# Performance work log

Measured on AMD Instinct MI355X. Metric: run time of the kernel, lower is better.

Reference implementation:

```python
import jax, jax.numpy as jnp
import numpy as np

B, N, FEAT, HID, HEADS = 16, 1024, 512, 1024, 2

def setup_inputs() -> dict:
    key = jax.random.key(0)
    ks = jax.random.split(key, 20)
    s = 0.03
    d = {
        'Fs':  jax.random.normal(ks[0], (B, N, FEAT), jnp.float32),
        'Fq':  jax.random.normal(ks[1], (B, N, FEAT), jnp.float32),
        'Fms': jax.random.normal(ks[2], (B, N, FEAT), jnp.float32),
        'out_dim': N,
        'W1': jax.random.normal(ks[3], (FEAT, FEAT), jnp.float32) * s,
        'W2': jax.random.normal(ks[4], (FEAT, FEAT), jnp.float32) * s,
        'W3': jax.random.normal(ks[5], (FEAT, FEAT), jnp.float32) * s,
        'W4': jax.random.normal(ks[6], (FEAT, FEAT), jnp.float32) * s,
        'W5': jax.random.normal(ks[7], (FEAT, FEAT), jnp.float32) * s,
        'W6': jax.random.normal(ks[8], (FEAT, FEAT), jnp.float32) * s,
        'Wq': jax.random.normal(ks[9], (N, N), jnp.float32) * s,
        'Wk': jax.random.normal(ks[10], (N, N), jnp.float32) * s,
        'Wv': jax.random.normal(ks[11], (N, N), jnp.float32) * s,
        'ln_g': jnp.ones((N,), jnp.float32),
        'ln_b': jnp.zeros((N,), jnp.float32),
        'ffn_w1': jax.random.normal(ks[12], (N, HID), jnp.float32) * s,
        'ffn_w2': jax.random.normal(ks[13], (HID, N), jnp.float32) * s,
        'ffn_ln_g': jnp.ones((N,), jnp.float32),
        'ffn_ln_b': jnp.zeros((N,), jnp.float32),
    }
    return d

def _layernorm(x, g, b, eps):
    mu = x.mean(-1, keepdims=True)
    var = x.var(-1, keepdims=True)
    return (x - mu) * jax.lax.rsqrt(var + eps) * g + b

def _affinity(a, b, Wa, Wb, cl):
    # softmax((a Wa)(b Wb)^T / sqrt(cl)) over last axis
    s = jnp.einsum('bnc,bmc->bnm', a @ Wa, b @ Wb) / jnp.sqrt(jnp.float32(cl))
    return jax.nn.softmax(s, axis=-1)

def reference(Fs, Fq, Fms, out_dim, W1, W2, W3, W4, W5, W6, Wq, Wk, Wv,
              ln_g, ln_b, ffn_w1, ffn_w2, ffn_ln_g, ffn_ln_b):
    ass = _affinity(Fms, Fms, W1, W2, Fms.shape[2])   # [B,N,N]
    asq = _affinity(Fs, Fq, W3, W4, Fs.shape[2])      # [B,N,N]
    aqq = _affinity(Fq, Fq, W5, W6, Fq.shape[2])      # [B,N,N]

    Q, K, V = asq @ Wq, ass @ Wk, asq @ Wv            # [B,N,C], C=N
    Bb, Nn, C = Q.shape
    g = C // HEADS
    def heads(x):
        return x.reshape(Bb, Nn, HEADS, g).transpose(0, 2, 1, 3)  # [B,h,N,g]
    Qs, Ks, Vs = heads(Q), heads(K), heads(V)
    attn = jax.nn.softmax(jnp.einsum('bhqg,bhkg->bhqk', Qs, Ks) / jnp.sqrt(jnp.float32(g)), axis=-1)
    o = jnp.einsum('bhqk,bhkg->bhqg', attn, Vs)
    o = o.transpose(0, 2, 1, 3).reshape(Bb, Nn, C)

    x = _layernorm(o + aqq, ln_g, ln_b, 1e-5)
    y = jnp.maximum(x @ ffn_w1, 0.0) @ ffn_w2 + x     # dropout = identity (eval)
    y = _layernorm(y, ffn_ln_g, ffn_ln_b, 1e-6)
    return y
```

## Files before the change

kernel.cpp:

```cpp
#include <hip/hip_runtime.h>
#include <cstdint>

static constexpr long long Bb = 16, Nn = 1024, FE = 512;
static constexpr long long BN = Bb * Nn;
static constexpr long long E1e = BN * FE;
static constexpr long long E2n = BN * Nn;

static constexpr long long O_WT  = 0;
static constexpr long long SZ_W512 = FE * FE * 2;
static constexpr long long O_WQT = O_WT + 6 * SZ_W512;
static constexpr long long SZ_W1K = Nn * Nn * 2;
static constexpr long long O_WKT = O_WQT + SZ_W1K;
static constexpr long long O_WVT = O_WKT + SZ_W1K;
static constexpr long long O_F1T = O_WVT + SZ_W1K;
static constexpr long long O_F2T = O_F1T + SZ_W1K;
static constexpr long long O_SLOTS = O_F2T + SZ_W1K;
static constexpr long long SLOT = E2n * 2;
static constexpr long long O_S0 = O_SLOTS;
static constexpr long long O_S1 = O_S0 + SLOT;
static constexpr long long O_S2 = O_S1 + SLOT;
static constexpr long long O_E0 = O_S2 + SLOT;
static constexpr long long O_E1 = O_E0 + SLOT;
static constexpr long long O_E2 = O_E1 + SLOT;
static constexpr long long WS_NEED = O_E2 + SLOT;
static constexpr long long O_FMSB = O_E1;
static constexpr long long O_FSB  = O_E1 + E1e * 2;
static constexpr long long O_FQB  = O_E2;
static constexpr long long O_C2   = O_E2 + E1e * 2;

typedef __attribute__((ext_vector_type(8))) short short8;
typedef __attribute__((ext_vector_type(4))) float f32x4;

static __device__ __forceinline__ unsigned short f2bf(float f) {
  union { float f; unsigned u; } x; x.f = f;
  unsigned r = x.u + 0x7FFFu + ((x.u >> 16) & 1u);
  return (unsigned short)(r >> 16);
}
static __device__ __forceinline__ float bf2f(unsigned short h) {
  union { unsigned u; float f; } x; x.u = ((unsigned)h) << 16; return x.f;
}
static __device__ __forceinline__ void gload16(const void* g, void* l) {
  __builtin_amdgcn_global_load_lds(
      (const __attribute__((address_space(1))) unsigned int*)g,
      (__attribute__((address_space(3))) unsigned int*)l, 16, 0, 0);
}

template <int EP>
__global__ __launch_bounds__(512, 2) void gemm256(
    const unsigned short* __restrict__ A, long long sA, long long hA, int lda,
    const unsigned short* __restrict__ B, long long sB, long long hB, int ldb,
    void* __restrict__ Cv, long long sC, long long hC, int ldc,
    const void* __restrict__ Rv, long long sR, int K) {
  extern __shared__ unsigned short lds[];
  const int tid = threadIdx.x;
  const int lane = tid & 63;
  const int wave = tid >> 6;
  const int wm = wave >> 2, wn = wave & 3;
  const int lrow = lane & 15, quad = lane >> 4;

  const int gx = gridDim.x;
  const int nxy = gx * gridDim.y;
  const int nwg = nxy * gridDim.z;
  int wg = blockIdx.x + gx * blockIdx.y + nxy * blockIdx.z;
  wg = (wg & 7) * (nwg >> 3) + (wg >> 3);
  const int bz = wg / nxy;
  const int rem = wg - bz * nxy;
  const int by = rem / gx;
  const int bx = rem - by * gx;
  const int z1 = bz & 15, z2 = bz >> 4;

  const long long bm = (long long)bx * 256;
  const long long bn = (long long)by * 256;
  const unsigned short* Ab = A + z1 * sA + z2 * hA + bm * lda;
  const unsigned short* Bp = B + z1 * sB + z2 * hB + bn * ldb;

  const int srow = tid >> 2;
  const int scol = ((tid & 3) ^ ((tid >> 3) & 3)) * 8;
  unsigned short* ldst = lds + tid * 8;

  auto STAGE = [&](int tt) {
    unsigned short* d = ldst + (tt & 3) * 16384;
    const long long ko = (long long)tt * 32 + scol;
    gload16(Ab + (long long)srow * lda + ko, d);
    gload16(Ab + (long long)(srow + 128) * lda + ko, d + 4096);
    gload16(Bp + (long long)srow * ldb + ko, d + 8192);
    gload16(Bp + (long long)(srow + 128) * ldb + ko, d + 12288);
  };

  const int swq = (quad ^ ((lrow >> 1) & 3)) * 8;
  const int a_off = (wm * 128 + lrow) * 32 + swq;
  const int b_off = 8192 + (wn * 64 + lrow) * 32 + swq;

  f32x4 acc[8][4];
#pragma unroll
  for (int m = 0; m < 8; ++m)
#pragma unroll
    for (int n = 0; n < 4; ++n) acc[m][n] = (f32x4){0.f, 0.f, 0.f, 0.f};

  auto COMPUTE = [&](int tt) {
    const unsigned short* lb = lds + (tt & 3) * 16384;
    short8 af[8], bfr[4];
#pragma unroll
    for (int m = 0; m < 8; ++m) af[m] = *(const short8*)&lb[a_off + m * 512];
#pragma unroll
    for (int n = 0; n < 4; ++n) bfr[n] = *(const short8*)&lb[b_off + n * 512];
    __builtin_amdgcn_s_setprio(1);
#pragma unroll
    for (int m = 0; m < 8; ++m)
#pragma unroll
      for (int n = 0; n < 4; ++n)
        acc[m][n] = __builtin_amdgcn_mfma_f32_16x16x32_bf16(af[m], bfr[n], acc[m][n], 0, 0, 0);
    __builtin_amdgcn_s_setprio(0);
  };

  const int nt = K >> 5;
  STAGE(0); STAGE(1); STAGE(2);
  int t = 0;
  for (; t < nt - 3; ++t) {
    STAGE(t + 3);
    asm volatile("s_waitcnt vmcnt(12)" ::: "memory");
    __builtin_amdgcn_s_barrier();
    COMPUTE(t);
    __builtin_amdgcn_s_barrier();
  }
  asm volatile("s_waitcnt vmcnt(8)" ::: "memory");
  __builtin_amdgcn_s_barrier();
  COMPUTE(t); ++t;
  asm volatile("s_waitcnt vmcnt(4)" ::: "memory");
  __builtin_amdgcn_s_barrier();
  COMPUTE(t); ++t;
  asm volatile("s_waitcnt vmcnt(0)" ::: "memory");
  __builtin_amdgcn_s_barrier();
  COMPUTE(t);

  const long long cm = bm + wm * 128, cn = bn + wn * 64;
  const long long cz = z1 * sC + z2 * hC;
#pragma unroll
  for (int mt = 0; mt < 8; ++mt) {
#pragma unroll
    for (int ntl = 0; ntl < 4; ++ntl) {
      long long col = cn + ntl * 16 + lrow;
      long long row0 = cm + mt * 16 + quad * 4;
#pragma unroll
      for (int r = 0; r < 4; ++r) {
        long long row = row0 + r;
        float v = acc[mt][ntl][r];
        long long idx = cz + row * ldc + col;
        if (EP == 1) ((unsigned short*)Cv)[idx] = f2bf(v);
        else if (EP == 2) ((unsigned short*)Cv)[idx] = f2bf(v > 0.f ? v : 0.f);
        else {
          float rr = bf2f(((const unsigned short*)Rv)[z1 * sR + row * ldc + col]);
          ((float*)Cv)[idx] = v + rr;
        }
      }
    }
  }
}

__global__ __launch_bounds__(256) void cast3_k(const float* __restrict__ i0,
                                               const float* __restrict__ i1,
                                               const float* __restrict__ i2,
                                               unsigned short* o0, unsigned short* o1,
                                               unsigned short* o2) {
  const float* in = (blockIdx.y == 0) ? i0 : (blockIdx.y == 1) ? i1 : i2;
  unsigned short* out = (blockIdx.y == 0) ? o0 : (blockIdx.y == 1) ? o1 : o2;
  long long i = (long long)blockIdx.x * 256 + threadIdx.x;
  float4 v = ((const float4*)in)[i];
  ushort4 o; o.x = f2bf(v.x); o.y = f2bf(v.y); o.z = f2bf(v.z); o.w = f2bf(v.w);
  ((ushort4*)out)[i] = o;
}

__global__ __launch_bounds__(256) void tcast6_k(const float* p0, const float* p1,
                                                const float* p2, const float* p3,
                                                const float* p4, const float* p5,
                                                unsigned short* outb, int rows, int cols) {
  const float* src[6] = {p0, p1, p2, p3, p4, p5};
  const float* in = src[blockIdx.z];
  unsigned short* out = outb + (long long)blockIdx.z * rows * cols;
  __shared__ float t[32][33];
  const int c0 = blockIdx.x * 32, r0 = blockIdx.y * 32;
  const int tx = threadIdx.x, ty = threadIdx.y;
#pragma unroll
  for (int i = 0; i < 4; ++i) {
    int r = r0 + ty + i * 8;
    t[ty + i * 8][tx] = in[(long long)r * cols + c0 + tx];
  }
  __syncthreads();
#pragma unroll
  for (int i = 0; i < 4; ++i) {
    int c = c0 + ty + i * 8;
    out[(long long)c * rows + r0 + tx] = f2bf(t[tx][ty + i * 8]);
  }
}

__global__ __launch_bounds__(256) void softmax_bf(unsigned short* __restrict__ S, float scale) {
  __shared__ float redA[4], redB[4];
  const long long row = blockIdx.x;
  const int t = threadIdx.x, wave = t >> 6, lane = t & 63;
  ushort4 u = ((ushort4*)(S + row * 1024))[t];
  float v0 = bf2f(u.x) * scale, v1 = bf2f(u.y) * scale, v2 = bf2f(u.z) * scale, v3 = bf2f(u.w) * scale;
  float m = fmaxf(fmaxf(v0, v1), fmaxf(v2, v3));
#pragma unroll
  for (int o = 32; o; o >>= 1) m = fmaxf(m, __shfl_down(m, o));
  if (lane == 0) redA[wave] = m;
  __syncthreads();
  m = fmaxf(fmaxf(redA[0], redA[1]), fmaxf(redA[2], redA[3]));
  float e0 = __expf(v0 - m), e1 = __expf(v1 - m), e2 = __expf(v2 - m), e3 = __expf(v3 - m);
  float s = e0 + e1 + e2 + e3;
#pragma unroll
  for (int o = 32; o; o >>= 1) s += __shfl_down(s, o);
  if (lane == 0) redB[wave] = s;
  __syncthreads();
  s = redB[0] + redB[1] + redB[2] + redB[3];
  float inv = 1.f / s;
  ushort4 ob; ob.x = f2bf(e0 * inv); ob.y = f2bf(e1 * inv); ob.z = f2bf(e2 * inv); ob.w = f2bf(e3 * inv);
  ((ushort4*)(S + row * 1024))[t] = ob;
}

__global__ __launch_bounds__(256) void ln1_k(const unsigned short* __restrict__ O,
                                             const unsigned short* __restrict__ Aq,
                                             const float* __restrict__ g, const float* __restrict__ b,
                                             unsigned short* __restrict__ xb) {
  __shared__ float redA[4], redB[4];
  const long long row = blockIdx.x;
  const int t = threadIdx.x, wave = t >> 6, lane = t & 63;
  ushort4 ou = ((const ushort4*)(O + row * 1024))[t];
  ushort4 au = ((const ushort4*)(Aq + row * 1024))[t];
  float v0 = bf2f(ou.x) + bf2f(au.x), v1 = bf2f(ou.y) + bf2f(au.y);
  float v2 = bf2f(ou.z) + bf2f(au.z), v3 = bf2f(ou.w) + bf2f(au.w);
  float s = v0 + v1 + v2 + v3;
  float q = v0 * v0 + v1 * v1 + v2 * v2 + v3 * v3;
#pragma unroll
  for (int o = 32; o; o >>= 1) { s += __shfl_down(s, o); q += __shfl_down(q, o); }
  if (lane == 0) { redA[wave] = s; redB[wave] = q; }
  __syncthreads();
  float S = redA[0] + redA[1] + redA[2] + redA[3];
  float Q = redB[0] + redB[1] + redB[2] + redB[3];
  float mu = S * (1.f / 1024.f);
  float var = Q * (1.f / 1024.f) - mu * mu;
  float rs = rsqrtf(var + 1e-5f);
  float4 gg = ((const float4*)g)[t], bbv = ((const float4*)b)[t];
  ushort4 ob;
  ob.x = f2bf((v0 - mu) * rs * gg.x + bbv.x);
  ob.y = f2bf((v1 - mu) * rs * gg.y + bbv.y);
  ob.z = f2bf((v2 - mu) * rs * gg.z + bbv.z);
  ob.w = f2bf((v3 - mu) * rs * gg.w + bbv.w);
  ((ushort4*)(xb + row * 1024))[t] = ob;
}

__global__ __launch_bounds__(256) void ln2_k(const float* __restrict__ Y,
                                             const float* __restrict__ g, const float* __restrict__ b,
                                             float* __restrict__ out, float eps) {
  __shared__ float redA[4], redB[4];
  const long long row = blockIdx.x;
  const int t = threadIdx.x, wave = t >> 6, lane = t & 63;
  float4 v = ((const float4*)(Y + row * 1024))[t];
  float s = v.x + v.y + v.z + v.w;
  float q = v.x * v.x + v.y * v.y + v.z * v.z + v.w * v.w;
#pragma unroll
  for (int o = 32; o; o >>= 1) { s += __shfl_down(s, o); q += __shfl_down(q, o); }
  if (lane == 0) { redA[wave] = s; redB[wave] = q; }
  __syncthreads();
  float S = redA[0] + redA[1] + redA[2] + redA[3];
  float Q = redB[0] + redB[1] + redB[2] + redB[3];
  float mu = S * (1.f / 1024.f);
  float var = Q * (1.f / 1024.f) - mu * mu;
  float rs = rsqrtf(var + eps);
  float4 gg = ((const float4*)g)[t], bbv = ((const float4*)b)[t];
  float4 o;
  o.x = (v.x - mu) * rs * gg.x + bbv.x;
  o.y = (v.y - mu) * rs * gg.y + bbv.y;
  o.z = (v.z - mu) * rs * gg.z + bbv.z;
  o.w = (v.w - mu) * rs * gg.w + bbv.w;
  ((float4*)(out + row * 1024))[t] = o;
}

extern "C" void kernel_launch(void* const* d_in, const int* in_sizes, int n_in,
                              void* d_out, int out_size, void* d_ws, size_t ws_size,
                              hipStream_t stream) {
  (void)in_sizes; (void)n_in; (void)out_size;
  if (ws_size < (size_t)WS_NEED) return;

  static int attr_once = []() {
    (void)hipFuncSetAttribute(reinterpret_cast<const void*>(&gemm256<1>),
                              hipFuncAttributeMaxDynamicSharedMemorySize, 131072);
    (void)hipFuncSetAttribute(reinterpret_cast<const void*>(&gemm256<2>),
                              hipFuncAttributeMaxDynamicSharedMemorySize, 131072);
    (void)hipFuncSetAttribute(reinterpret_cast<const void*>(&gemm256<3>),
                              hipFuncAttributeMaxDynamicSharedMemorySize, 131072);
    return 0;
  }();
  (void)attr_once;

  const float* Fs  = (const float*)d_in[0];
  const float* Fq  = (const float*)d_in[1];
  const float* Fms = (const float*)d_in[2];
  const float* Wm[6] = {(const float*)d_in[4], (const float*)d_in[5], (const float*)d_in[6],
                        (const float*)d_in[7], (const float*)d_in[8], (const float*)d_in[9]};
  const float* Wq = (const float*)d_in[10];
  const float* Wk = (const float*)d_in[11];
  const float* Wv = (const float*)d_in[12];
  const float* ln_g = (const float*)d_in[13];
  const float* ln_b = (const float*)d_in[14];
  const float* fw1 = (const float*)d_in[15];
  const float* fw2 = (const float*)d_in[16];
  const float* fg = (const float*)d_in[17];
  const float* fb = (const float*)d_in[18];
  float* out = (float*)d_out;
  uint8_t* ws = (uint8_t*)d_ws;
  auto U16 = [&](long long off) { return (unsigned short*)(ws + off); };

  const float inv_sqrt512 = 0.04419417382415922f;
  dim3 blk(256);

  auto gemm = [&](int ep, const unsigned short* A, long long sA, long long hA, int lda,
                  const unsigned short* B, long long sB, long long hB, int ldb,
                  void* C, long long sC, long long hC, int ldc, const void* R, long long sR,
                  int M, int N, int K, int batch) {
    dim3 g(M / 256, N / 256, batch);
    dim3 b(512);
    switch (ep) {
      case 1: gemm256<1><<<g, b, 131072, stream>>>(A, sA, hA, lda, B, sB, hB, ldb, C, sC, hC, ldc, R, sR, K); break;
      case 2: gemm256<2><<<g, b, 131072, stream>>>(A, sA, hA, lda, B, sB, hB, ldb, C, sC, hC, ldc, R, sR, K); break;
      default: gemm256<3><<<g, b, 131072, stream>>>(A, sA, hA, lda, B, sB, hB, ldb, C, sC, hC, ldc, R, sR, K); break;
    }
  };

  tcast6_k<<<dim3(16, 16, 6), dim3(32, 8), 0, stream>>>(
      Wm[0], Wm[1], Wm[2], Wm[3], Wm[4], Wm[5], U16(O_WT), 512, 512);
  tcast6_k<<<dim3(32, 32, 5), dim3(32, 8), 0, stream>>>(
      Wq, Wk, Wv, fw1, fw2, fw2 , U16(O_WQT), 1024, 1024);
  cast3_k<<<dim3(E1e / 4 / 256, 3), blk, 0, stream>>>(
      Fs, Fq, Fms, U16(O_FSB), U16(O_FQB), U16(O_FMSB));

  gemm(1, U16(O_FMSB), 16777216, 0, 512, U16(O_WT), 786432, 0, 512,
       U16(O_S0), 16777216, 0, 1024, nullptr, 0, (int)BN, 1024, 512, 2);
  gemm(1, U16(O_S0), Nn * 1024, 0, 1024, U16(O_S0) + 512, Nn * 1024, 0, 1024,
       U16(O_E0), Nn * Nn, 0, 1024, nullptr, 0, 1024, 1024, 512, (int)Bb);
  gemm(1, U16(O_FSB), 8388608, 0, 512, U16(O_WT + 2 * SZ_W512), 786432, 0, 512,
       U16(O_C2), -58720256LL, 0, 512, nullptr, 0, (int)BN, 512, 512, 2);
  gemm(1, U16(O_C2), Nn * 512, 0, 512, U16(O_S1), Nn * 1024, 0, 1024,
       U16(O_E1), Nn * Nn, 0, 1024, nullptr, 0, 1024, 1024, 512, (int)Bb);
  gemm(1, U16(O_S1) + 512, Nn * 1024, 0, 1024, U16(O_S2), Nn * 512, 0, 512,
       U16(O_E2), Nn * Nn, 0, 1024, nullptr, 0, 1024, 1024, 512, (int)Bb);
  softmax_bf<<<dim3(3 * BN), blk, 0, stream>>>(U16(O_E0), inv_sqrt512);

  const unsigned short* assB = U16(O_E0);

  gemm(1, assB, Nn * Nn, E2n, 1024,
       U16(O_WKT), 0, -(long long)(SZ_W1K / 2), 1024,
       U16(O_S1), Nn * 1024, -(long long)E2n, 1024,
       nullptr, 0, 1024, 1024, 1024, 32);
  gemm(1, U16(O_WVT), 0, 0, 1024, U16(O_E1), Nn * Nn, 0, 1024, U16(O_S2), Nn * Nn, 0, 1024,
       nullptr, 0, 1024, 1024, 1024, (int)Bb);

  gemm(1, U16(O_S0), Nn * 1024, 512, 1024, U16(O_S1), Nn * 1024, 512, 1024,
       U16(O_E0), Nn * Nn, 16 * Nn * Nn, 1024, nullptr, 0, 1024, 1024, 512, 32);
  softmax_bf<<<dim3(2 * BN), blk, 0, stream>>>(U16(O_E0), inv_sqrt512);

  gemm(1, U16(O_E0), Nn * Nn, 16 * Nn * Nn, 1024, U16(O_S2), Nn * Nn, 512 * 1024, 1024,
       U16(O_S0), Nn * 1024, 512, 1024, nullptr, 0, 1024, 512, 1024, 32);

  ln1_k<<<dim3(BN), blk, 0, stream>>>(U16(O_S0), U16(O_E2), ln_g, ln_b, U16(O_S1));

  gemm(2, U16(O_S1), 0, 0, 1024, U16(O_F1T), 0, 0, 1024, U16(O_S2), 0, 0, 1024,
       nullptr, 0, (int)BN, 1024, 1024, 1);

  gemm(3, U16(O_S2), 0, 0, 1024, U16(O_F2T), 0, 0, 1024, out, 0, 0, 1024,
       U16(O_S1), 0, (int)BN, 1024, 1024, 1);

  ln2_k<<<dim3(BN), blk, 0, stream>>>(out, fg, fb, out, 1e-6f);
}
```

Measured before the change: 723.4 us.

## Load B fragments directly from global into registers, halve LDS staging

The GEMM kernel now stages only the A tile through LDS. Each wave loads its B MFMA fragments directly from global memory into registers, using a double-buffered register ping-pong across k-steps. The loop is unrolled by two and the tail is rewritten to match, and dynamic LDS drops from 128KB to 64KB, which could allow higher occupancy. In exchange, B rows are no longer shared through LDS, so global/L2 traffic for B rises, and the direct loads are narrow and strided per lane.

```diff
diff --git a/kernel.cpp b/kernel.cpp
--- a/kernel.cpp
+++ b/kernel.cpp
@@ -77,19 +77,20 @@
   const int srow = tid >> 2;
   const int scol = ((tid & 3) ^ ((tid >> 3) & 3)) * 8;
   unsigned short* ldst = lds + tid * 8;
-
   auto STAGE = [&](int tt) {
-    unsigned short* d = ldst + (tt & 3) * 16384;
+    unsigned short* d = ldst + (tt & 3) * 8192;
     const long long ko = (long long)tt * 32 + scol;
     gload16(Ab + (long long)srow * lda + ko, d);
     gload16(Ab + (long long)(srow + 128) * lda + ko, d + 4096);
-    gload16(Bp + (long long)srow * ldb + ko, d + 8192);
-    gload16(Bp + (long long)(srow + 128) * ldb + ko, d + 12288);
   };
 
   const int swq = (quad ^ ((lrow >> 1) & 3)) * 8;
   const int a_off = (wm * 128 + lrow) * 32 + swq;
-  const int b_off = 8192 + (wn * 64 + lrow) * 32 + swq;
+
+  const unsigned short* Bf[4];
+#pragma unroll
+  for (int f = 0; f < 4; ++f)
+    Bf[f] = Bp + (long long)(wn * 64 + f * 16 + lrow) * ldb + quad * 8;
 
   f32x4 acc[8][4];
 #pragma unroll
@@ -97,41 +98,63 @@
 #pragma unroll
     for (int n = 0; n < 4; ++n) acc[m][n] = (f32x4){0.f, 0.f, 0.f, 0.f};
 
-  auto COMPUTE = [&](int tt) {
-    const unsigned short* lb = lds + (tt & 3) * 16384;
-    short8 af[8], bfr[4];
+  short8 af[8], be[4], bo[4];
+  auto READ_A = [&](int tt) {
+    const unsigned short* lb = lds + (tt & 3) * 8192;
 #pragma unroll
     for (int m = 0; m < 8; ++m) af[m] = *(const short8*)&lb[a_off + m * 512];
-#pragma unroll
-    for (int n = 0; n < 4; ++n) bfr[n] = *(const short8*)&lb[b_off + n * 512];
+  };
+  auto LOADB = [&](int tt, short8* dst) {
+#pragma unroll
+    for (int f = 0; f < 4; ++f)
+      dst[f] = *(const short8*)(Bf[f] + (long long)tt * 32);
+  };
+  auto MFMAC = [&](const short8* bb) {
     __builtin_amdgcn_s_setprio(1);
 #pragma unroll
     for (int m = 0; m < 8; ++m)
 #pragma unroll
       for (int n = 0; n < 4; ++n)
-        acc[m][n] = __builtin_amdgcn_mfma_f32_16x16x32_bf16(af[m], bfr[n], acc[m][n], 0, 0, 0);
+        acc[m][n] = __builtin_amdgcn_mfma_f32_16x16x32_bf16(af[m], bb[n], acc[m][n], 0, 0, 0);
     __builtin_amdgcn_s_setprio(0);
   };
 
   const int nt = K >> 5;
   STAGE(0); STAGE(1); STAGE(2);
+  LOADB(0, be);
+  asm volatile("s_waitcnt vmcnt(8)" ::: "memory");
+  __builtin_amdgcn_s_barrier();
   int t = 0;
-  for (; t < nt - 3; ++t) {
+  for (; t < nt - 6; t += 2) {
+    READ_A(t);
     STAGE(t + 3);
-    asm volatile("s_waitcnt vmcnt(12)" ::: "memory");
+    LOADB(t + 1, bo);
+    MFMAC(be);
+    asm volatile("s_waitcnt vmcnt(6)" ::: "memory");
     __builtin_amdgcn_s_barrier();
-    COMPUTE(t);
+    READ_A(t + 1);
+    STAGE(t + 4);
+    LOADB(t + 2, be);
+    MFMAC(bo);
+    asm volatile("s_waitcnt vmcnt(6)" ::: "memory");
     __builtin_amdgcn_s_barrier();
   }
-  asm volatile("s_waitcnt vmcnt(8)" ::: "memory");
-  __builtin_amdgcn_s_barrier();
-  COMPUTE(t); ++t;
+  READ_A(nt - 6); STAGE(nt - 3); LOADB(nt - 5, bo); MFMAC(be);
+  asm volatile("s_waitcnt vmcnt(6)" ::: "memory");
+  __builtin_amdgcn_s_barrier();
+  READ_A(nt - 5); STAGE(nt - 2); LOADB(nt - 4, be); MFMAC(bo);
+  asm volatile("s_waitcnt vmcnt(6)" ::: "memory");
+  __builtin_amdgcn_s_barrier();
+  READ_A(nt - 4); STAGE(nt - 1); LOADB(nt - 3, bo); MFMAC(be);
+  asm volatile("s_waitcnt vmcnt(6)" ::: "memory");
+  __builtin_amdgcn_s_barrier();
+  READ_A(nt - 3); LOADB(nt - 2, be); MFMAC(bo);
   asm volatile("s_waitcnt vmcnt(4)" ::: "memory");
   __builtin_amdgcn_s_barrier();
-  COMPUTE(t); ++t;
-  asm volatile("s_waitcnt vmcnt(0)" ::: "memory");
-  __builtin_amdgcn_s_barrier();
-  COMPUTE(t);
+  READ_A(nt - 2); LOADB(nt - 1, bo); MFMAC(be);
+  asm volatile("s_waitcnt vmcnt(4)" ::: "memory");
+  __builtin_amdgcn_s_barrier();
+  READ_A(nt - 1); MFMAC(bo);
 
   const long long cm = bm + wm * 128, cn = bn + wn * 64;
   const long long cz = z1 * sC + z2 * hC;
@@ -283,11 +306,11 @@
 
   static int attr_once = []() {
     (void)hipFuncSetAttribute(reinterpret_cast<const void*>(&gemm256<1>),
-                              hipFuncAttributeMaxDynamicSharedMemorySize, 131072);
+                              hipFuncAttributeMaxDynamicSharedMemorySize, 65536);
     (void)hipFuncSetAttribute(reinterpret_cast<const void*>(&gemm256<2>),
-                              hipFuncAttributeMaxDynamicSharedMemorySize, 131072);
+                              hipFuncAttributeMaxDynamicSharedMemorySize, 65536);
     (void)hipFuncSetAttribute(reinterpret_cast<const void*>(&gemm256<3>),
-                              hipFuncAttributeMaxDynamicSharedMemorySize, 131072);
+                              hipFuncAttributeMaxDynamicSharedMemorySize, 65536);
     return 0;
   }();
   (void)attr_once;
@@ -320,9 +343,9 @@
     dim3 g(M / 256, N / 256, batch);
     dim3 b(512);
     switch (ep) {
-      case 1: gemm256<1><<<g, b, 131072, stream>>>(A, sA, hA, lda, B, sB, hB, ldb, C, sC, hC, ldc, R, sR, K); break;
-      case 2: gemm256<2><<<g, b, 131072, stream>>>(A, sA, hA, lda, B, sB, hB, ldb, C, sC, hC, ldc, R, sR, K); break;
-      default: gemm256<3><<<g, b, 131072, stream>>>(A, sA, hA, lda, B, sB, hB, ldb, C, sC, hC, ldc, R, sR, K); break;
+      case 1: gemm256<1><<<g, b, 65536, stream>>>(A, sA, hA, lda, B, sB, hB, ldb, C, sC, hC, ldc, R, sR, K); break;
+      case 2: gemm256<2><<<g, b, 65536, stream>>>(A, sA, hA, lda, B, sB, hB, ldb, C, sC, hC, ldc, R, sR, K); break;
+      default: gemm256<3><<<g, b, 65536, stream>>>(A, sA, hA, lda, B, sB, hB, ldb, C, sC, hC, ldc, R, sR, K); break;
     }
   };
 
```

After: 865.0 us. 19.6% more time.
